# Optimization experiments

Hardware: AMD Instinct MI355X
Metric: run time of the kernel (lower is better)

Reference implementation:

```python
import jax, jax.numpy as jnp
import numpy as np

B, G, D = 4096, 256, 32
N_TYPES, N_IN, N_OUT = 4, 8, 4
CE = G * D  # 8192 circuit-embed dim
ACTIVITY_FACTOR = 0.5
TEMPERATURE = 1.0


def _mlp_params(key, dims):
    ps = []
    for i, (fi, fo) in enumerate(zip(dims[:-1], dims[1:])):
        k1, k2, key = jax.random.split(key, 3)
        lim = 1.0 / np.sqrt(fi)
        ps.append(jax.random.uniform(k1, (fi, fo), jnp.float32, -lim, lim))
        ps.append(jax.random.uniform(k2, (fo,), jnp.float32, -lim, lim))
    return ps


def setup_inputs() -> dict:
    key = jax.random.key(0)
    ks = jax.random.split(key, 10)
    inp = {
        'gate_types': jax.random.randint(ks[0], (B, G), 0, N_TYPES, jnp.int32),
        'connections': jax.random.uniform(ks[1], (B, G, G), jnp.float32),
        'inputs': jax.random.normal(ks[2], (B, N_IN), jnp.float32),
        'outputs': jax.random.normal(ks[3], (B, N_OUT), jnp.float32),
        'emb': jax.random.normal(ks[4], (N_TYPES, D), jnp.float32),
    }
    pw1, pb1, pw2, pb2 = _mlp_params(ks[5], [CE, 128, 1])
    dw1, db1, dw2, db2 = _mlp_params(ks[6], [CE, 128, 1])
    nw1, nb1, nw2, nb2 = _mlp_params(ks[7], [CE, 128, 1])
    cw1, cb1, cw2, cb2, cw3, cb3 = _mlp_params(ks[8], [CE + N_IN + N_OUT, 256, 128, 1])
    inp.update(pw1=pw1, pb1=pb1, pw2=pw2, pb2=pb2,
               dw1=dw1, db1=db1, dw2=dw2, db2=db2,
               nw1=nw1, nb1=nb1, nw2=nw2, nb2=nb2,
               cw1=cw1, cb1=cb1, cw2=cw2, cb2=cb2, cw3=cw3, cb3=cb3)
    return inp


def _head(x, w1, b1, w2, b2, act):
    h = jax.nn.relu(x @ w1 + b1)
    return act(h @ w2 + b2)[:, 0]


def reference(gate_types, connections, inputs, outputs, emb,
              pw1, pb1, pw2, pb2, dw1, db1, dw2, db2,
              nw1, nb1, nw2, nb2, cw1, cb1, cw2, cb2, cw3, cb3):
    # circuit embedding: [B, G, D] -> [B, G*D]
    ce = emb[gate_types].reshape(B, CE)

    # energy = softplus head + dynamic power from connection count
    base_power = _head(ce, pw1, pb1, pw2, pb2, jax.nn.softplus)
    num_conn = connections.sum(axis=(1, 2))  # [B]
    energy = base_power + ACTIVITY_FACTOR * num_conn * 0.1

    # gate-type entropy via fixed-vocab bincount (replaces per-batch torch.unique)
    counts = jnp.sum(jax.nn.one_hot(gate_types, N_TYPES, dtype=jnp.float32), axis=1)  # [B, 4]
    probs = counts / jnp.float32(G)
    gate_ent = -jnp.sum(jnp.where(probs > 0, probs * jnp.log2(jnp.where(probs > 0, probs, 1.0)), 0.0), axis=1)

    # connection (binary) entropy of density
    dens = num_conn / jnp.float32(G * G)
    valid = (dens > 0) & (dens < 1)
    d_safe = jnp.clip(dens, 1e-12, 1 - 1e-12)
    conn_ent = jnp.where(valid, -d_safe * jnp.log2(d_safe) - (1 - d_safe) * jnp.log2(1 - d_safe), 0.0)
    entropy = gate_ent + conn_ent

    # thermal stability
    stability = _head(ce, nw1, nb1, nw2, nb2, jax.nn.sigmoid) * jnp.exp(jnp.float32(-TEMPERATURE))

    # correctness: 3-layer MLP on [circuit_embed, inputs, outputs]
    full = jnp.concatenate([ce, inputs, outputs], axis=1)
    h = jax.nn.relu(full @ cw1 + cb1)
    h = jax.nn.relu(h @ cw2 + cb2)
    correctness = jax.nn.sigmoid(h @ cw3 + cb3)[:, 0]

    delay = _head(ce, dw1, db1, dw2, db2, jax.nn.softplus)

    return energy, entropy, stability, correctness, delay
```

## Files before the change

### kernel.cpp

```cpp
#include <hip/hip_runtime.h>
#include <math.h>

#define BB 4096
#define GG 256
#define DD 32
#define CE 8192

__device__ __forceinline__ float softplusf_(float x) {
    return fmaxf(x, 0.0f) + log1pf(expf(-fabsf(x)));
}
__device__ __forceinline__ float sigmoidf_(float x) {
    return 1.0f / (1.0f + expf(-x));
}

__global__ void build_tables(const float* __restrict__ emb,
                             const float* __restrict__ pw1,
                             const float* __restrict__ dw1,
                             const float* __restrict__ nw1,
                             const float* __restrict__ cw1,
                             float* __restrict__ tp, float* __restrict__ td,
                             float* __restrict__ tn, float* __restrict__ tc) {
    const int g  = blockIdx.x;
    const int ty = blockIdx.y;
    const int h  = threadIdx.x;
    __shared__ float se[DD];
    if (h < DD) se[h] = emb[ty * DD + h];
    __syncthreads();
    float ap = 0.f, ad = 0.f, an = 0.f, ac = 0.f;
    const int rbase = g * DD;
#pragma unroll
    for (int d = 0; d < DD; ++d) {
        const float e = se[d];
        const int r = rbase + d;
        if (h < 128) {
            ap = fmaf(e, pw1[r * 128 + h], ap);
            ad = fmaf(e, dw1[r * 128 + h], ad);
            an = fmaf(e, nw1[r * 128 + h], an);
        }
        ac = fmaf(e, cw1[r * 256 + h], ac);
    }
    const int row = ty * GG + g;
    if (h < 128) {
        tp[row * 128 + h] = ap;
        td[row * 128 + h] = ad;
        tn[row * 128 + h] = an;
    }
    tc[row * 256 + h] = ac;
}

__global__ __launch_bounds__(256) void circuit_main(
    const int*   __restrict__ gate_types,
    const float* __restrict__ connections,
    const float* __restrict__ inputs,
    const float* __restrict__ outputs,
    const float* __restrict__ pb1, const float* __restrict__ pw2, const float* __restrict__ pb2,
    const float* __restrict__ db1, const float* __restrict__ dw2, const float* __restrict__ db2,
    const float* __restrict__ nb1, const float* __restrict__ nw2, const float* __restrict__ nb2,
    const float* __restrict__ cw1, const float* __restrict__ cb1,
    const float* __restrict__ cw2, const float* __restrict__ cb2,
    const float* __restrict__ cw3, const float* __restrict__ cb3,
    const float* __restrict__ tp, const float* __restrict__ td,
    const float* __restrict__ tn, const float* __restrict__ tc,
    float* __restrict__ out)
{
    const int b = blockIdx.x;
    const int t = threadIdx.x;

    __shared__ int   s_gt[GG];
    __shared__ int   s_cnt[4];
    __shared__ float s_io[12];
    __shared__ float s_red[96];
    __shared__ float s_hc[256];
    __shared__ float s_wred[4];
    __shared__ float s_logit[3];
    __shared__ float s_cred[2];

    if (t < 4) s_cnt[t] = 0;
    __syncthreads();
    {
        const int gt = gate_types[b * GG + t];
        s_gt[t] = gt;
        atomicAdd(&s_cnt[gt], 1);
        if (t < 8)       s_io[t] = inputs[b * 8 + t];
        else if (t < 12) s_io[t] = outputs[b * 4 + (t - 8)];
    }
    __syncthreads();

    const float4* tbl4;
    int W4, off;
    if (t < 32)       { tbl4 = (const float4*)tp; W4 = 32; off = t; }
    else if (t < 64)  { tbl4 = (const float4*)td; W4 = 32; off = t - 32; }
    else if (t < 96)  { tbl4 = (const float4*)tn; W4 = 32; off = t - 64; }
    else              { tbl4 = (const float4*)tc; W4 = 64; off = t - 96; }
    const bool active = (t < 160);

    const float4* connb = (const float4*)(connections + (size_t)b * (GG * GG));

    float ax = 0.f, ay = 0.f, az = 0.f, aw = 0.f;
    float cs = 0.f;
#pragma unroll 4
    for (int g = 0; g < GG; ++g) {
        const int gt = s_gt[g];
        if (active) {
            const float4 v = tbl4[(gt * GG + g) * W4 + off];
            ax += v.x; ay += v.y; az += v.z; aw += v.w;
        }
        if ((g & 3) == 0) {
            const float4 c = connb[(g >> 2) * 256 + t];
            cs += c.x + c.y + c.z + c.w;
        }
    }

#pragma unroll
    for (int o = 32; o > 0; o >>= 1) cs += __shfl_down(cs, o, 64);
    if ((t & 63) == 0) s_wred[t >> 6] = cs;

    if (t < 96) {
        const int hb = (t & 31) * 4;
        const float* b1 = (t < 32) ? pb1 : (t < 64) ? db1 : nb1;
        const float* w2 = (t < 32) ? pw2 : (t < 64) ? dw2 : nw2;
        const float h0 = fmaxf(ax + b1[hb + 0], 0.f);
        const float h1 = fmaxf(ay + b1[hb + 1], 0.f);
        const float h2 = fmaxf(az + b1[hb + 2], 0.f);
        const float h3 = fmaxf(aw + b1[hb + 3], 0.f);
        s_red[t] = h0 * w2[hb + 0] + h1 * w2[hb + 1] + h2 * w2[hb + 2] + h3 * w2[hb + 3];
    } else if (t < 160) {
        const int h = (t - 96) * 4;
#pragma unroll
        for (int j = 0; j < 12; ++j) {
            const float s = s_io[j];
            const float4 w = *(const float4*)&cw1[(size_t)(CE + j) * 256 + h];
            ax = fmaf(s, w.x, ax); ay = fmaf(s, w.y, ay);
            az = fmaf(s, w.z, az); aw = fmaf(s, w.w, aw);
        }
        s_hc[h + 0] = fmaxf(ax + cb1[h + 0], 0.f);
        s_hc[h + 1] = fmaxf(ay + cb1[h + 1], 0.f);
        s_hc[h + 2] = fmaxf(az + cb1[h + 2], 0.f);
        s_hc[h + 3] = fmaxf(aw + cb1[h + 3], 0.f);
    }
    __syncthreads();

    if (t < 128) {
        float a = 0.f;
#pragma unroll 8
        for (int h = 0; h < 256; ++h) a = fmaf(s_hc[h], cw2[h * 128 + t], a);
        a = fmaxf(a + cb2[t], 0.f) * cw3[t];
#pragma unroll
        for (int o = 32; o > 0; o >>= 1) a += __shfl_down(a, o, 64);
        if ((t & 63) == 0) s_cred[t >> 6] = a;
    }
    if (t == 128) { float s = 0.f; for (int i = 0;  i < 32; ++i) s += s_red[i];      s_logit[0] = s + pb2[0]; }
    if (t == 129) { float s = 0.f; for (int i = 32; i < 64; ++i) s += s_red[i];      s_logit[1] = s + db2[0]; }
    if (t == 130) { float s = 0.f; for (int i = 64; i < 96; ++i) s += s_red[i];      s_logit[2] = s + nb2[0]; }
    __syncthreads();

    if (t == 0) {
        const float num_conn = s_wred[0] + s_wred[1] + s_wred[2] + s_wred[3];
        const float lp = s_logit[0], ld = s_logit[1], ln = s_logit[2];
        const float lc = s_cred[0] + s_cred[1] + cb3[0];

        const float energy = softplusf_(lp) + 0.05f * num_conn;

        float gate_ent = 0.f;
#pragma unroll
        for (int k = 0; k < 4; ++k) {
            const float c = (float)s_cnt[k];
            if (c > 0.f) {
                const float p = c * (1.0f / 256.0f);
                gate_ent -= p * log2f(p);
            }
        }
        const float dens = num_conn * (1.0f / 65536.0f);
        float conn_ent = 0.f;
        if (dens > 0.f && dens < 1.f) {
            const float dsf = fminf(fmaxf(dens, 1e-12f), 1.f - 1e-12f);
            conn_ent = -dsf * log2f(dsf) - (1.f - dsf) * log2f(1.f - dsf);
        }

        out[b]           = energy;
        out[BB + b]      = gate_ent + conn_ent;
        out[2 * BB + b]  = sigmoidf_(ln) * 0.36787944117144233f;
        out[3 * BB + b]  = sigmoidf_(lc);
        out[4 * BB + b]  = softplusf_(ld);
    }
}

extern "C" void kernel_launch(void* const* d_in, const int* in_sizes, int n_in,
                              void* d_out, int out_size, void* d_ws, size_t ws_size,
                              hipStream_t stream) {
    const int*   gate_types  = (const int*)  d_in[0];
    const float* connections = (const float*)d_in[1];
    const float* inputs      = (const float*)d_in[2];
    const float* outputs     = (const float*)d_in[3];
    const float* emb         = (const float*)d_in[4];
    const float* pw1 = (const float*)d_in[5];
    const float* pb1 = (const float*)d_in[6];
    const float* pw2 = (const float*)d_in[7];
    const float* pb2 = (const float*)d_in[8];
    const float* dw1 = (const float*)d_in[9];
    const float* db1 = (const float*)d_in[10];
    const float* dw2 = (const float*)d_in[11];
    const float* db2 = (const float*)d_in[12];
    const float* nw1 = (const float*)d_in[13];
    const float* nb1 = (const float*)d_in[14];
    const float* nw2 = (const float*)d_in[15];
    const float* nb2 = (const float*)d_in[16];
    const float* cw1 = (const float*)d_in[17];
    const float* cb1 = (const float*)d_in[18];
    const float* cw2 = (const float*)d_in[19];
    const float* cb2 = (const float*)d_in[20];
    const float* cw3 = (const float*)d_in[21];
    const float* cb3 = (const float*)d_in[22];

    float* ws = (float*)d_ws;
    float* tp = ws;
    float* td = tp + 4 * 256 * 128;
    float* tn = td + 4 * 256 * 128;
    float* tc = tn + 4 * 256 * 128;

    build_tables<<<dim3(256, 4), 256, 0, stream>>>(emb, pw1, dw1, nw1, cw1, tp, td, tn, tc);

    circuit_main<<<BB, 256, 0, stream>>>(
        gate_types, connections, inputs, outputs,
        pb1, pw2, pb2, db1, dw2, db2, nb1, nw2, nb2,
        cw1, cb1, cw2, cb2, cw3, cb3,
        tp, td, tn, tc,
        (float*)d_out);
}
```

Measured before the change: 1.659 ms.

## Interleave lookup tables into one row-major table and batch connection loads per chunk

```diff
diff --git a/kernel.cpp b/kernel.cpp
--- a/kernel.cpp
+++ b/kernel.cpp
@@ -18,8 +18,7 @@
                              const float* __restrict__ dw1,
                              const float* __restrict__ nw1,
                              const float* __restrict__ cw1,
-                             float* __restrict__ tp, float* __restrict__ td,
-                             float* __restrict__ tn, float* __restrict__ tc) {
+                             float* __restrict__ tall) {
     const int g  = blockIdx.x;
     const int ty = blockIdx.y;
     const int h  = threadIdx.x;
@@ -39,13 +38,13 @@
         }
         ac = fmaf(e, cw1[r * 256 + h], ac);
     }
-    const int row = ty * GG + g;
+    float* dst = tall + (size_t)(((ty << 8) + g)) * 640;
     if (h < 128) {
-        tp[row * 128 + h] = ap;
-        td[row * 128 + h] = ad;
-        tn[row * 128 + h] = an;
-    }
-    tc[row * 256 + h] = ac;
+        dst[h]       = ap;
+        dst[128 + h] = ad;
+        dst[256 + h] = an;
+    }
+    dst[384 + h] = ac;
 }
 
 __global__ __launch_bounds__(256) void circuit_main(
@@ -59,8 +58,7 @@
     const float* __restrict__ cw1, const float* __restrict__ cb1,
     const float* __restrict__ cw2, const float* __restrict__ cb2,
     const float* __restrict__ cw3, const float* __restrict__ cb3,
-    const float* __restrict__ tp, const float* __restrict__ td,
-    const float* __restrict__ tn, const float* __restrict__ tc,
+    const float* __restrict__ tall,
     float* __restrict__ out)
 {
     const int b = blockIdx.x;
@@ -79,36 +77,36 @@
     __syncthreads();
     {
         const int gt = gate_types[b * GG + t];
-        s_gt[t] = gt;
         atomicAdd(&s_cnt[gt], 1);
+        s_gt[t] = ((gt << 8) + t) * 160;
         if (t < 8)       s_io[t] = inputs[b * 8 + t];
         else if (t < 12) s_io[t] = outputs[b * 4 + (t - 8)];
     }
     __syncthreads();
 
-    const float4* tbl4;
-    int W4, off;
-    if (t < 32)       { tbl4 = (const float4*)tp; W4 = 32; off = t; }
-    else if (t < 64)  { tbl4 = (const float4*)td; W4 = 32; off = t - 32; }
-    else if (t < 96)  { tbl4 = (const float4*)tn; W4 = 32; off = t - 64; }
-    else              { tbl4 = (const float4*)tc; W4 = 64; off = t - 96; }
+    const float4* tall4 = (const float4*)tall;
+    const float4* connb = (const float4*)(connections + (size_t)b * (GG * GG));
     const bool active = (t < 160);
-
-    const float4* connb = (const float4*)(connections + (size_t)b * (GG * GG));
 
     float ax = 0.f, ay = 0.f, az = 0.f, aw = 0.f;
     float cs = 0.f;
-#pragma unroll 4
-    for (int g = 0; g < GG; ++g) {
-        const int gt = s_gt[g];
+
+    for (int gc = 0; gc < GG; gc += 16) {
+        float4 c0 = connb[((gc >> 2) + 0) * 256 + t];
+        float4 c1 = connb[((gc >> 2) + 1) * 256 + t];
+        float4 c2 = connb[((gc >> 2) + 2) * 256 + t];
+        float4 c3 = connb[((gc >> 2) + 3) * 256 + t];
         if (active) {
-            const float4 v = tbl4[(gt * GG + g) * W4 + off];
-            ax += v.x; ay += v.y; az += v.z; aw += v.w;
-        }
-        if ((g & 3) == 0) {
-            const float4 c = connb[(g >> 2) * 256 + t];
-            cs += c.x + c.y + c.z + c.w;
-        }
+#pragma unroll
+            for (int gg = 0; gg < 16; ++gg) {
+                const float4 v = tall4[s_gt[gc + gg] + t];
+                ax += v.x; ay += v.y; az += v.z; aw += v.w;
+            }
+        }
+        cs += (c0.x + c0.y) + (c0.z + c0.w);
+        cs += (c1.x + c1.y) + (c1.z + c1.w);
+        cs += (c2.x + c2.y) + (c2.z + c2.w);
+        cs += (c3.x + c3.y) + (c3.z + c3.w);
     }
 
 #pragma unroll
@@ -212,18 +210,14 @@
     const float* cw3 = (const float*)d_in[21];
     const float* cb3 = (const float*)d_in[22];
 
-    float* ws = (float*)d_ws;
-    float* tp = ws;
-    float* td = tp + 4 * 256 * 128;
-    float* tn = td + 4 * 256 * 128;
-    float* tc = tn + 4 * 256 * 128;
-
-    build_tables<<<dim3(256, 4), 256, 0, stream>>>(emb, pw1, dw1, nw1, cw1, tp, td, tn, tc);
+    float* tall = (float*)d_ws;
+
+    build_tables<<<dim3(256, 4), 256, 0, stream>>>(emb, pw1, dw1, nw1, cw1, tall);
 
     circuit_main<<<BB, 256, 0, stream>>>(
         gate_types, connections, inputs, outputs,
         pb1, pw2, pb2, db1, dw2, db2, nb1, nw2, nb2,
         cw1, cb1, cw2, cb2, cw3, cb3,
-        tp, td, tn, tc,
+        tall,
         (float*)d_out);
 }
```

After: 1.489 ms. -10.3%, faster.
